# Kernel optimization log

Hardware: AMD Instinct MI355X
Metric: run time of the kernel (lower is better)

The kernel has to match this reference:

```python
import jax, jax.numpy as jnp
import numpy as np

B = 8192      # batch
J = 32        # slots = 30 goal joints + traj + heading
C = 4         # target_cond_dim (3 input features + 1 validity flag)
D = 256       # splited_dim = latent_dim // J = 8192 // 32


def setup_inputs() -> dict:
    key = jax.random.key(0)
    k0, k1, k2, k3, k4, k5 = jax.random.split(key, 6)
    s1 = 1.0 / np.sqrt(C)  # torch Linear default init bound
    s2 = 1.0 / np.sqrt(D)
    return {
        "input": jax.random.normal(k0, (B, J, 3), jnp.float32),
        "validity": jax.random.randint(k1, (B, J), 0, 2, jnp.int32),
        # per-slot MLP params, stacked over the slot axis J
        "W1": jax.random.uniform(k2, (J, C, D), jnp.float32, -s1, s1),
        "b1": jax.random.uniform(k3, (J, D), jnp.float32, -s1, s1),
        "W2": jax.random.uniform(k4, (J, D, D), jnp.float32, -s2, s2),
        "b2": jax.random.uniform(k5, (J, D), jnp.float32, -s2, s2),
    }


def reference(input, validity, W1, b1, W2, b2):
    # mlp_input = cat([input, validity], -1) -> [B, J, 4]
    x = jnp.concatenate([input, validity[..., None].astype(input.dtype)], axis=-1)
    # per-slot Linear(4, D): batched over slots via einsum (replaces the Python loop)
    h = jnp.einsum('bjc,jcd->bjd', x, W1) + b1          # [B, J, D]
    h = jax.nn.silu(h)
    h = jnp.einsum('bjd,jde->bje', h, W2) + b2          # [B, J, D]
    # torch.cat(mlp_splits, dim=-1) == reshape since slots are contiguous
    return h.reshape(B, J * D)                           # [B, latent_dim]
```

## Files before the change

kernel.cpp:

```cpp
#include <hip/hip_runtime.h>

typedef short bf16x8 __attribute__((ext_vector_type(8)));
typedef float f32x4 __attribute__((ext_vector_type(4)));

#define AS1 __attribute__((address_space(1)))
#define AS3 __attribute__((address_space(3)))

__device__ __forceinline__ unsigned short f2bf(float f) {
  unsigned int u = __builtin_bit_cast(unsigned int, f);
  return (unsigned short)((u + 0x8000u) >> 16);
}

__global__ __launch_bounds__(256) void prep_w2t(const float* __restrict__ W2,
                                                unsigned char* __restrict__ w2t) {
  const int s = blockIdx.x;
  const int jc = blockIdx.y;
  const int j = jc >> 1, ch = jc & 1;
  const int t = threadIdx.x;
  __shared__ unsigned short lds[64 * 136];

  const float* src = W2 + (size_t)j * 65536 + (size_t)(s * 64) * 256 + ch * 128;
#pragma unroll
  for (int i = 0; i < 8; ++i) {
    const int idx4 = i * 256 + t;
    const int kk = idx4 >> 5;
    const int n4 = (idx4 & 31) << 2;
    const float4 v = *reinterpret_cast<const float4*>(src + kk * 256 + n4);
    unsigned short* p = &lds[kk * 136 + n4];
    p[0] = f2bf(v.x); p[1] = f2bf(v.y); p[2] = f2bf(v.z); p[3] = f2bf(v.w);
  }
  __syncthreads();

  unsigned char* dst = w2t + (((size_t)jc * 4 + s) << 14);
#pragma unroll
  for (int i = 0; i < 4; ++i) {
    const int slot = i * 256 + t;
    const int n = slot >> 3, u = slot & 7;
    const int kk0 = (u ^ (n & 7)) << 3;
    unsigned int w[4];
#pragma unroll
    for (int q = 0; q < 4; ++q) {
      const unsigned int lo = lds[(kk0 + 2 * q + 0) * 136 + n];
      const unsigned int hi = lds[(kk0 + 2 * q + 1) * 136 + n];
      w[q] = lo | (hi << 16);
    }
    *reinterpret_cast<uint4*>(dst + slot * 16) = make_uint4(w[0], w[1], w[2], w[3]);
  }
}

__global__ __launch_bounds__(512, 4) void fused_mlp(
    const float* __restrict__ input, const int* __restrict__ validity,
    const float* __restrict__ W1, const float* __restrict__ b1,
    const float* __restrict__ b2, const unsigned char* __restrict__ w2t,
    float* __restrict__ out) {
  __shared__ __align__(16) unsigned char smem[70656];
  const int bx = blockIdx.x;
  const int by = blockIdx.y;
  const int j = by >> 1, ch = by & 1;
  const int tid = threadIdx.x;
  const int wid = tid >> 6;
  const int lane = tid & 63;
  const int l15 = lane & 15, lg = lane >> 4;
  const int rowbase = (bx << 8) + (wid << 5);

  float xr[2][4];
#pragma unroll
  for (int mf = 0; mf < 2; ++mf) {
    const int row = rowbase + mf * 16 + l15;
    const float* ip = input + ((size_t)row * 32 + j) * 3;
    xr[mf][0] = ip[0]; xr[mf][1] = ip[1]; xr[mf][2] = ip[2];
    xr[mf][3] = (float)validity[row * 32 + j];
  }
  const float* b2j = b2 + (j << 8) + (ch << 7) + l15;
  float b2v[8];
#pragma unroll
  for (int nf = 0; nf < 8; ++nf) b2v[nf] = b2j[nf << 4];
  float4 wst = make_float4(0.f, 0.f, 0.f, 0.f);
  if (tid < 320) {
    const float* ws = (tid < 256) ? (W1 + (j << 10) + (tid << 2))
                                  : (b1 + (j << 8) + ((tid - 256) << 2));
    wst = *reinterpret_cast<const float4*>(ws);
  }

  const unsigned char* w2tj = w2t + ((size_t)by << 16);
#pragma unroll
  for (int it = 0; it < 8; ++it) {
    const int off = ((it << 3) + wid) << 10;
    __builtin_amdgcn_global_load_lds(
        (const AS1 unsigned int*)(w2tj + off + lane * 16),
        (AS3 unsigned int*)(smem + off), 16, 0, 0);
  }

  if (tid < 320) *reinterpret_cast<float4*>(smem + 65536 + (tid << 4)) = wst;

  f32x4 acc[2][8];
#pragma unroll
  for (int nf = 0; nf < 8; ++nf) {
    acc[0][nf] = f32x4{b2v[nf], b2v[nf], b2v[nf], b2v[nf]};
    acc[1][nf] = acc[0][nf];
  }

  asm volatile("s_waitcnt lgkmcnt(0)" ::: "memory");
  __builtin_amdgcn_s_barrier();

  const unsigned char* w1base = smem + 65536 + (lg << 5);
  const int q0 = (lg << 4) ^ ((l15 & 7) << 4);
  const unsigned char* rA = smem + l15 * 128 + q0;
  const unsigned char* rB = smem + l15 * 128 + (q0 ^ 64);

  const size_t colbase = (size_t)(j << 8) + (ch << 7) + l15;

#pragma unroll
  for (int s = 0; s < 4; ++s) {
    bf16x8 af[2][2];
#pragma unroll
    for (int kf2 = 0; kf2 < 2; ++kf2) {
      const int kf = 2 * s + kf2;
#pragma unroll
      for (int half = 0; half < 2; ++half) {
        const int im = kf * 128 + half * 16;
        const f32x4 w0 = *reinterpret_cast<const f32x4*>(w1base + im);
        const f32x4 w1v = *reinterpret_cast<const f32x4*>(w1base + 1024 + im);
        const f32x4 w2v = *reinterpret_cast<const f32x4*>(w1base + 2048 + im);
        const f32x4 w3v = *reinterpret_cast<const f32x4*>(w1base + 3072 + im);
        const f32x4 bb = *reinterpret_cast<const f32x4*>(w1base + 4096 + im);
#pragma unroll
        for (int mf = 0; mf < 2; ++mf) {
#pragma unroll
          for (int i = 0; i < 4; ++i) {
            float z = bb[i];
            z = fmaf(xr[mf][0], w0[i], z);
            z = fmaf(xr[mf][1], w1v[i], z);
            z = fmaf(xr[mf][2], w2v[i], z);
            z = fmaf(xr[mf][3], w3v[i], z);
            const float h = z * __builtin_amdgcn_rcpf(1.0f + __expf(-z));
            af[kf2][mf][half * 4 + i] = (short)f2bf(h);
          }
        }
      }
    }

    if (s == 0)      asm volatile("s_waitcnt vmcnt(6)" ::: "memory");
    else if (s == 1) asm volatile("s_waitcnt vmcnt(4)" ::: "memory");
    else if (s == 2) asm volatile("s_waitcnt vmcnt(2)" ::: "memory");
    else             asm volatile("s_waitcnt vmcnt(0)" ::: "memory");
    __builtin_amdgcn_s_barrier();

    const int base = s << 14;
#pragma unroll
    for (int nf = 0; nf < 8; ++nf) {
      const bf16x8 bf0 = *reinterpret_cast<const bf16x8*>(rA + base + nf * 2048);
      const bf16x8 bf1 = *reinterpret_cast<const bf16x8*>(rB + base + nf * 2048);
      acc[0][nf] = __builtin_amdgcn_mfma_f32_16x16x32_bf16(af[0][0], bf0, acc[0][nf], 0, 0, 0);
      acc[1][nf] = __builtin_amdgcn_mfma_f32_16x16x32_bf16(af[0][1], bf0, acc[1][nf], 0, 0, 0);
      acc[0][nf] = __builtin_amdgcn_mfma_f32_16x16x32_bf16(af[1][0], bf1, acc[0][nf], 0, 0, 0);
      acc[1][nf] = __builtin_amdgcn_mfma_f32_16x16x32_bf16(af[1][1], bf1, acc[1][nf], 0, 0, 0);
    }
  }

#pragma unroll
  for (int mf = 0; mf < 2; ++mf) {
#pragma unroll
    for (int r = 0; r < 4; ++r) {
      const int row = rowbase + mf * 16 + (lg << 2) + r;
      float* pr = out + (size_t)row * 8192 + colbase;
#pragma unroll
      for (int nf = 0; nf < 8; ++nf) pr[nf << 4] = acc[mf][nf][r];
    }
  }
}

extern "C" void kernel_launch(void* const* d_in, const int* in_sizes, int n_in,
                              void* d_out, int out_size, void* d_ws, size_t ws_size,
                              hipStream_t stream) {
  (void)in_sizes; (void)n_in; (void)out_size; (void)ws_size;
  const float* input    = (const float*)d_in[0];
  const int*   validity = (const int*)d_in[1];
  const float* W1       = (const float*)d_in[2];
  const float* b1       = (const float*)d_in[3];
  const float* W2       = (const float*)d_in[4];
  const float* b2       = (const float*)d_in[5];
  float* out = (float*)d_out;
  unsigned char* w2t = (unsigned char*)d_ws;

  prep_w2t<<<dim3(4, 64), 256, 0, stream>>>(W2, w2t);
  fused_mlp<<<dim3(32, 64), 512, 0, stream>>>(input, validity, W1, b1, b2, w2t, out);
}
```

Baseline: 89.46 us.

## Persistent blocks loop over four row tiles reusing staged W2 slice

The grid shrinks from 2048 to 512 blocks, and each block now processes four 256-row tiles for its slot/column-half. The 64KB W2 slice and W1/b1 therefore load into LDS once and are reused four times. b2 moves into LDS, the next tile's inputs are prefetched during the last k-step, and the SiLU A-fragment computation is split per k-fragment to lower register pressure. The risks are fewer blocks hiding latency over 256 CUs and serialized tiles inside each block.

```diff
diff --git a/kernel.cpp b/kernel.cpp
--- a/kernel.cpp
+++ b/kernel.cpp
@@ -48,37 +48,62 @@
   }
 }
 
+__device__ __forceinline__ void jit_af(const unsigned char* w1base,
+                                       const float xr[2][4], int kf,
+                                       bf16x8 af[2]) {
+#pragma unroll
+  for (int half = 0; half < 2; ++half) {
+    const int im = kf * 128 + half * 16;
+    const f32x4 w0 = *reinterpret_cast<const f32x4*>(w1base + im);
+    const f32x4 w1v = *reinterpret_cast<const f32x4*>(w1base + 1024 + im);
+    const f32x4 w2v = *reinterpret_cast<const f32x4*>(w1base + 2048 + im);
+    const f32x4 w3v = *reinterpret_cast<const f32x4*>(w1base + 3072 + im);
+    const f32x4 bb = *reinterpret_cast<const f32x4*>(w1base + 4096 + im);
+#pragma unroll
+    for (int mf = 0; mf < 2; ++mf) {
+#pragma unroll
+      for (int i = 0; i < 4; ++i) {
+        float z = bb[i];
+        z = fmaf(xr[mf][0], w0[i], z);
+        z = fmaf(xr[mf][1], w1v[i], z);
+        z = fmaf(xr[mf][2], w2v[i], z);
+        z = fmaf(xr[mf][3], w3v[i], z);
+        const float h = z * __builtin_amdgcn_rcpf(1.0f + __expf(-z));
+        af[mf][half * 4 + i] = (short)f2bf(h);
+      }
+    }
+  }
+}
+
 __global__ __launch_bounds__(512, 4) void fused_mlp(
     const float* __restrict__ input, const int* __restrict__ validity,
     const float* __restrict__ W1, const float* __restrict__ b1,
     const float* __restrict__ b2, const unsigned char* __restrict__ w2t,
     float* __restrict__ out) {
-  __shared__ __align__(16) unsigned char smem[70656];
-  const int bx = blockIdx.x;
-  const int by = blockIdx.y;
+  __shared__ __align__(16) unsigned char smem[71168];
+  const int bid = blockIdx.x;
+  const int by = bid & 63;
+  const int grp = bid >> 6;
   const int j = by >> 1, ch = by & 1;
   const int tid = threadIdx.x;
   const int wid = tid >> 6;
   const int lane = tid & 63;
   const int l15 = lane & 15, lg = lane >> 4;
-  const int rowbase = (bx << 8) + (wid << 5);
-
+
+  const int row0 = (grp << 10) + (wid << 5);
+  const float* ipA = input + ((size_t)(row0 + l15) * 32 + j) * 3;
+  const float* ipB = ipA + 16 * 32 * 3;
+  const int* vpA = validity + (row0 + l15) * 32 + j;
+  const int* vpB = vpA + 16 * 32;
   float xr[2][4];
-#pragma unroll
-  for (int mf = 0; mf < 2; ++mf) {
-    const int row = rowbase + mf * 16 + l15;
-    const float* ip = input + ((size_t)row * 32 + j) * 3;
-    xr[mf][0] = ip[0]; xr[mf][1] = ip[1]; xr[mf][2] = ip[2];
-    xr[mf][3] = (float)validity[row * 32 + j];
-  }
-  const float* b2j = b2 + (j << 8) + (ch << 7) + l15;
-  float b2v[8];
-#pragma unroll
-  for (int nf = 0; nf < 8; ++nf) b2v[nf] = b2j[nf << 4];
+  xr[0][0] = ipA[0]; xr[0][1] = ipA[1]; xr[0][2] = ipA[2]; xr[0][3] = (float)*vpA;
+  xr[1][0] = ipB[0]; xr[1][1] = ipB[1]; xr[1][2] = ipB[2]; xr[1][3] = (float)*vpB;
+
   float4 wst = make_float4(0.f, 0.f, 0.f, 0.f);
-  if (tid < 320) {
+  if (tid < 352) {
     const float* ws = (tid < 256) ? (W1 + (j << 10) + (tid << 2))
-                                  : (b1 + (j << 8) + ((tid - 256) << 2));
+                    : (tid < 320) ? (b1 + (j << 8) + ((tid - 256) << 2))
+                                  : (b2 + (j << 8) + (ch << 7) + ((tid - 320) << 2));
     wst = *reinterpret_cast<const float4*>(ws);
   }
 
@@ -91,81 +116,86 @@
         (AS3 unsigned int*)(smem + off), 16, 0, 0);
   }
 
-  if (tid < 320) *reinterpret_cast<float4*>(smem + 65536 + (tid << 4)) = wst;
-
-  f32x4 acc[2][8];
-#pragma unroll
-  for (int nf = 0; nf < 8; ++nf) {
-    acc[0][nf] = f32x4{b2v[nf], b2v[nf], b2v[nf], b2v[nf]};
-    acc[1][nf] = acc[0][nf];
-  }
+  if (tid < 352) *reinterpret_cast<float4*>(smem + 65536 + (tid << 4)) = wst;
 
   asm volatile("s_waitcnt lgkmcnt(0)" ::: "memory");
   __builtin_amdgcn_s_barrier();
 
   const unsigned char* w1base = smem + 65536 + (lg << 5);
+  const unsigned char* b2base = smem + 70656 + (l15 << 2);
   const int q0 = (lg << 4) ^ ((l15 & 7) << 4);
   const unsigned char* rA = smem + l15 * 128 + q0;
   const unsigned char* rB = smem + l15 * 128 + (q0 ^ 64);
 
   const size_t colbase = (size_t)(j << 8) + (ch << 7) + l15;
-
-#pragma unroll
-  for (int s = 0; s < 4; ++s) {
-    bf16x8 af[2][2];
-#pragma unroll
-    for (int kf2 = 0; kf2 < 2; ++kf2) {
-      const int kf = 2 * s + kf2;
-#pragma unroll
-      for (int half = 0; half < 2; ++half) {
-        const int im = kf * 128 + half * 16;
-        const f32x4 w0 = *reinterpret_cast<const f32x4*>(w1base + im);
-        const f32x4 w1v = *reinterpret_cast<const f32x4*>(w1base + 1024 + im);
-        const f32x4 w2v = *reinterpret_cast<const f32x4*>(w1base + 2048 + im);
-        const f32x4 w3v = *reinterpret_cast<const f32x4*>(w1base + 3072 + im);
-        const f32x4 bb = *reinterpret_cast<const f32x4*>(w1base + 4096 + im);
-#pragma unroll
-        for (int mf = 0; mf < 2; ++mf) {
-#pragma unroll
-          for (int i = 0; i < 4; ++i) {
-            float z = bb[i];
-            z = fmaf(xr[mf][0], w0[i], z);
-            z = fmaf(xr[mf][1], w1v[i], z);
-            z = fmaf(xr[mf][2], w2v[i], z);
-            z = fmaf(xr[mf][3], w3v[i], z);
-            const float h = z * __builtin_amdgcn_rcpf(1.0f + __expf(-z));
-            af[kf2][mf][half * 4 + i] = (short)f2bf(h);
-          }
-        }
-      }
-    }
-
-    if (s == 0)      asm volatile("s_waitcnt vmcnt(6)" ::: "memory");
-    else if (s == 1) asm volatile("s_waitcnt vmcnt(4)" ::: "memory");
-    else if (s == 2) asm volatile("s_waitcnt vmcnt(2)" ::: "memory");
-    else             asm volatile("s_waitcnt vmcnt(0)" ::: "memory");
-    __builtin_amdgcn_s_barrier();
-
-    const int base = s << 14;
+  float* outbase = out + (size_t)(row0 + (lg << 2)) * 8192 + colbase;
+
+  f32x4 acc[2][8];
+  bf16x8 af[2];
+  float xrn[2][4];
+
+#pragma unroll 1
+  for (int t = 0; t < 4; ++t) {
 #pragma unroll
     for (int nf = 0; nf < 8; ++nf) {
-      const bf16x8 bf0 = *reinterpret_cast<const bf16x8*>(rA + base + nf * 2048);
-      const bf16x8 bf1 = *reinterpret_cast<const bf16x8*>(rB + base + nf * 2048);
-      acc[0][nf] = __builtin_amdgcn_mfma_f32_16x16x32_bf16(af[0][0], bf0, acc[0][nf], 0, 0, 0);
-      acc[1][nf] = __builtin_amdgcn_mfma_f32_16x16x32_bf16(af[0][1], bf0, acc[1][nf], 0, 0, 0);
-      acc[0][nf] = __builtin_amdgcn_mfma_f32_16x16x32_bf16(af[1][0], bf1, acc[0][nf], 0, 0, 0);
-      acc[1][nf] = __builtin_amdgcn_mfma_f32_16x16x32_bf16(af[1][1], bf1, acc[1][nf], 0, 0, 0);
-    }
-  }
-
-#pragma unroll
-  for (int mf = 0; mf < 2; ++mf) {
-#pragma unroll
-    for (int r = 0; r < 4; ++r) {
-      const int row = rowbase + mf * 16 + (lg << 2) + r;
-      float* pr = out + (size_t)row * 8192 + colbase;
-#pragma unroll
-      for (int nf = 0; nf < 8; ++nf) pr[nf << 4] = acc[mf][nf][r];
+      const float b = *reinterpret_cast<const float*>(b2base + (nf << 6));
+      acc[0][nf] = f32x4{b, b, b, b};
+      acc[1][nf] = acc[0][nf];
+    }
+
+#pragma unroll
+    for (int s = 0; s < 4; ++s) {
+      if (s == 3 && t < 3) {
+        ipA += 24576; ipB += 24576; vpA += 8192; vpB += 8192;
+        xrn[0][0] = ipA[0]; xrn[0][1] = ipA[1]; xrn[0][2] = ipA[2];
+        xrn[0][3] = (float)*vpA;
+        xrn[1][0] = ipB[0]; xrn[1][1] = ipB[1]; xrn[1][2] = ipB[2];
+        xrn[1][3] = (float)*vpB;
+      }
+
+      jit_af(w1base, xr, 2 * s, af);
+
+      if (t == 0) {
+        if (s == 0)      asm volatile("s_waitcnt vmcnt(6)" ::: "memory");
+        else if (s == 1) asm volatile("s_waitcnt vmcnt(4)" ::: "memory");
+        else if (s == 2) asm volatile("s_waitcnt vmcnt(2)" ::: "memory");
+        else             asm volatile("s_waitcnt vmcnt(0)" ::: "memory");
+        __builtin_amdgcn_s_barrier();
+      }
+
+      const int base = s << 14;
+#pragma unroll
+      for (int nf = 0; nf < 8; ++nf) {
+        const bf16x8 bf0 = *reinterpret_cast<const bf16x8*>(rA + base + nf * 2048);
+        acc[0][nf] = __builtin_amdgcn_mfma_f32_16x16x32_bf16(af[0], bf0, acc[0][nf], 0, 0, 0);
+        acc[1][nf] = __builtin_amdgcn_mfma_f32_16x16x32_bf16(af[1], bf0, acc[1][nf], 0, 0, 0);
+      }
+
+      jit_af(w1base, xr, 2 * s + 1, af);
+#pragma unroll
+      for (int nf = 0; nf < 8; ++nf) {
+        const bf16x8 bf1 = *reinterpret_cast<const bf16x8*>(rB + base + nf * 2048);
+        acc[0][nf] = __builtin_amdgcn_mfma_f32_16x16x32_bf16(af[0], bf1, acc[0][nf], 0, 0, 0);
+        acc[1][nf] = __builtin_amdgcn_mfma_f32_16x16x32_bf16(af[1], bf1, acc[1][nf], 0, 0, 0);
+      }
+    }
+
+#pragma unroll
+    for (int mf = 0; mf < 2; ++mf) {
+#pragma unroll
+      for (int r = 0; r < 4; ++r) {
+        float* pr = outbase + (size_t)(mf * 16 + r) * 8192;
+#pragma unroll
+        for (int nf = 0; nf < 8; ++nf) pr[nf << 4] = acc[mf][nf][r];
+      }
+    }
+    outbase += (size_t)256 * 8192;
+
+    if (t < 3) {
+#pragma unroll
+      for (int mf = 0; mf < 2; ++mf)
+#pragma unroll
+        for (int c = 0; c < 4; ++c) xr[mf][c] = xrn[mf][c];
     }
   }
 }
@@ -184,5 +214,5 @@
   unsigned char* w2t = (unsigned char*)d_ws;
 
   prep_w2t<<<dim3(4, 64), 256, 0, stream>>>(W2, w2t);
-  fused_mlp<<<dim3(32, 64), 512, 0, stream>>>(input, validity, W1, b1, b2, w2t, out);
-}
+  fused_mlp<<<512, 512, 0, stream>>>(input, validity, W1, b1, b2, w2t, out);
+}
```

After: 114.5 us. 1.28x slower.
